# Performance work log

Measured on AMD Instinct MI355X. Metric: run time of the kernel, lower is better.

## Reference

```python
import jax, jax.numpy as jnp
import numpy as np

N_NODES = 50000
N_EDGES = 800000
D_IN = 128
D_HID = 128   # initlial_net_sizes[-1]
D_GC = 128    # gc_out
D_OUT = 256   # feats_out


def setup_inputs() -> dict:
    key = jax.random.key(0)
    ks = jax.random.split(key, 8)
    feats = jax.random.normal(ks[0], (N_NODES, D_IN), dtype=jnp.float32)
    edges = jax.random.randint(ks[1], (2, N_EDGES), 0, N_NODES, dtype=jnp.int64)
    batch = jnp.sort(jax.random.randint(ks[2], (N_NODES,), 0, 64, dtype=jnp.int64))
    s = 0.05
    W1 = jax.random.normal(ks[3], (D_IN, D_HID), dtype=jnp.float32) * s
    b1 = jnp.zeros((D_HID,), dtype=jnp.float32)
    Wg = jax.random.normal(ks[4], (D_HID, D_GC), dtype=jnp.float32) * s
    bg = jnp.zeros((D_GC,), dtype=jnp.float32)
    W2 = jax.random.normal(ks[5], (D_HID + D_GC, D_OUT), dtype=jnp.float32) * s
    b2 = jnp.zeros((D_OUT,), dtype=jnp.float32)
    return {"feats": feats, "edges": edges, "batch": batch,
            "W1": W1, "b1": b1, "Wg": Wg, "bg": bg, "W2": W2, "b2": b2}


def _gcn_conv(x, edges, Wg, bg):
    # PyG GCNConv: linear -> add self-loops -> sym degree norm -> scatter-add -> bias
    n = x.shape[0]
    x = x @ Wg                                   # [N, D_GC]
    loop = jnp.arange(n, dtype=edges.dtype)
    src = jnp.concatenate([edges[0], loop])      # message source (x_j)
    dst = jnp.concatenate([edges[1], loop])      # aggregation target
    deg = jax.ops.segment_sum(jnp.ones_like(dst, dtype=x.dtype), dst, num_segments=n)
    dinv = jnp.where(deg > 0, jax.lax.rsqrt(deg), 0.0)
    norm = dinv[src] * dinv[dst]                 # [E+N]
    msg = x[src] * norm[:, None]                 # [E+N, D_GC]
    out = jax.ops.segment_sum(msg, dst, num_segments=n)
    return out + bg


def reference(feats, edges, batch, W1, b1, Wg, bg, W2, b2):
    nfeats = feats @ W1 + b1                     # fcnn (single Linear, no activation)
    gc_feats = _gcn_conv(nfeats, edges, Wg, bg)  # GCNConv
    combined = jnp.concatenate([nfeats, gc_feats], axis=1) @ W2 + b2
    return (combined, edges, batch)
```

## Files before the change

### kernel.cpp

```cpp
#include <hip/hip_runtime.h>
#include <hip/hip_bf16.h>
#include <stdint.h>


#define NND 50000
#define NE  800000

typedef unsigned int u32;
typedef unsigned short u16;
typedef unsigned long long u64;
typedef short bf16x8 __attribute__((ext_vector_type(8)));
typedef float f32x4  __attribute__((ext_vector_type(4)));

#define OFF_CSR  12800000
#define OFF_RNK  13200000
#define OFF_ROW  13600000
#define OFF_DEG  13700004
#define OFF_DINV 13750004
#define OFF_WPK2 13800004
#define OFF_WPK1 13832772
#define OFF_WPKG 13840964

__device__ __forceinline__ float bf_lo(u32 u) { return __uint_as_float(u << 16); }
__device__ __forceinline__ float bf_hi(u32 u) { return __uint_as_float(u & 0xFFFF0000u); }
__device__ __forceinline__ unsigned short f2b(float f) {
    __hip_bfloat16 h = __float2bfloat16(f);
    return *(unsigned short*)&h;
}
__device__ __forceinline__ u32 pk2(float lo, float hi) {
    return ((u32)f2b(hi) << 16) | (u32)f2b(lo);
}

__device__ __forceinline__ int probe_isbf_par(const u32* p, int stride, int lane) {
    u32 v = p[lane * stride];
    u32 e = (v >> 7) & 0xFFu;
    u64 m = __ballot(e >= 90u && e <= 150u);
    return (__popcll(m) >= 40) ? 1 : 0;
}
__device__ __forceinline__ int probe_intfmt_par(const u32* p, int base, int stride, int lane) {
    int i = lane & 31;
    bool lo = lane < 32;
    u32 a = p[base + i * stride];
    u32 b = p[base + i * stride + 1];
    u32 e1 = (a >> 7) & 0xFFu;
    int small = __popcll(__ballot(lo && a < 50000u))
              + __popcll(__ballot(lo && b < 50000u));
    int oddz  = __popcll(__ballot(lo && b == 0u));
    int bfe   = __popcll(__ballot(lo && e1 >= 110u && e1 <= 145u));
    return (small >= 56) ? ((oddz >= 31) ? 1 : 0) : ((bfe >= 20) ? 3 : 2);
}

__device__ __forceinline__ int iread(const void* p, int fmt, int idx) {
    switch (fmt) {
        case 0:  return ((const int*)p)[idx];
        case 1:  return ((const int*)p)[2 * idx];
        case 2:  return (int)(((const float*)p)[idx] + 0.5f);
        default: return (int)(__bfloat162float(((const __hip_bfloat16*)p)[idx]) + 0.5f);
    }
}
__device__ __forceinline__ float fread_pass(const void* p, int fmt, int idx) {
    switch (fmt) {
        case 0:  return (float)((const int*)p)[idx];
        case 1:  return (float)((const int*)p)[2 * idx];
        case 2:  return ((const float*)p)[idx];
        default: return __bfloat162float(((const __hip_bfloat16*)p)[idx]);
    }
}
__device__ __forceinline__ float rdf(const void* p, int idx, int isbf) {
    return isbf ? __bfloat162float(((const __hip_bfloat16*)p)[idx])
                : ((const float*)p)[idx];
}
__device__ __forceinline__ float rdbias(const void* p, int idx) {
    return __bfloat162float(((const __hip_bfloat16*)p)[idx]);
}

__global__ __launch_bounds__(256) void k_pack(
    const void* W1, const void* Wg, const void* W2,
    u16* __restrict__ Wpk1, u16* __restrict__ Wpkg, u16* __restrict__ Wpk2,
    int* __restrict__ deg)
{
    int b = blockIdx.x, tid = threadIdx.x, lane = tid & 63;
    if (b < 64) {
        int wbf = probe_isbf_par((const u32*)W1, 127, lane);
        int idx = b * 256 + tid;
        int j = idx & 7, l = (idx >> 3) & 63, nt = (idx >> 9) & 7, kk = (idx >> 12) & 3;
        int k = kk * 32 + ((l >> 4) & 3) * 8 + j;
        int n = nt * 16 + (l & 15);
        Wpk1[idx] = f2b(rdf(W1, k * 128 + n, wbf));
    } else if (b < 128) {
        int wbf = probe_isbf_par((const u32*)Wg, 127, lane);
        int idx = (b - 64) * 256 + tid;
        int j = idx & 7, l = (idx >> 3) & 63, nt = (idx >> 9) & 7, kk = (idx >> 12) & 3;
        int k = kk * 32 + ((l >> 4) & 3) * 8 + j;
        int n = nt * 16 + (l & 15);
        Wpkg[idx] = f2b(rdf(Wg, k * 128 + n, wbf));
    } else if (b < 384) {
        int wbf = probe_isbf_par((const u32*)W2, 509, lane);
        int idx = (b - 128) * 256 + tid;
        int j = idx & 7, l = (idx >> 3) & 63, nt = (idx >> 9) & 15, kk = idx >> 13;
        int k = kk * 32 + ((l >> 4) & 3) * 8 + j;
        int n = nt * 16 + (l & 15);
        Wpk2[idx] = f2b(rdf(W2, k * 256 + n, wbf));
    } else {
        int idx = (b - 384) * 256 + tid;
        if (idx < 12500) ((int4*)deg)[idx] = make_int4(0, 0, 0, 0);
    }
}

__global__ __launch_bounds__(256) void k_degnfxp(
    const void* edges, const void* feats,
    const u32* __restrict__ Wpk1, const u32* __restrict__ Wpkg, const void* b1,
    int* __restrict__ deg, u16* __restrict__ rank16,
    float* __restrict__ out, int M)
{
    __shared__ alignas(16) u32 smem[2048 + 2176];
    int b = blockIdx.x, tid = threadIdx.x, lane = tid & 63;

    if (b < 3125) {
        int fmt = probe_intfmt_par((const u32*)edges, 0, 24992, lane);
        int e = b * 256 + tid;
        if (e < NE) {
            int s = iread(edges, fmt, e);
            int d = iread(edges, fmt, NE + e);
            if ((u32)s < (u32)NND && (u32)d < (u32)NND) {
                int r = atomicAdd(&deg[d], 1);
                rank16[e] = (u16)r;
            }
        }
        return;
    }

    int nb = b - 3125;
    int row0 = nb * 32;
    int w = tid >> 6;
    u32* sApk = smem;
    uint4* sApk4 = (uint4*)smem;
    u16* nfl  = (u16*)(smem + 2048);

    int fbf = probe_isbf_par((const u32*)feats, 997, lane);

    if (fbf) {
        const u32* fw = (const u32*)feats;
        for (int i4 = tid; i4 < 512; i4 += 256) {
            int l = i4 & 63, kk = (i4 >> 6) & 3, mt = (i4 >> 8) & 1;
            int m = mt * 16 + (l & 15);
            int k0b = kk * 32 + ((l >> 4) & 3) * 8;
            int row = row0 + m;
            uint4 v = make_uint4(0u, 0u, 0u, 0u);
            if (row < M) v = *(const uint4*)&fw[(size_t)row * 64 + (k0b >> 1)];
            sApk4[i4] = v;
        }
    } else {
        const float* ff = (const float*)feats;
        for (int i4 = tid; i4 < 512; i4 += 256) {
            int l = i4 & 63, kk = (i4 >> 6) & 3, mt = (i4 >> 8) & 1;
            int m = mt * 16 + (l & 15);
            int k0b = kk * 32 + ((l >> 4) & 3) * 8;
            int row = row0 + m;
            uint4 v = make_uint4(0u, 0u, 0u, 0u);
            if (row < M) {
                float4 fa = *(const float4*)&ff[(size_t)row * 128 + k0b];
                float4 fb = *(const float4*)&ff[(size_t)row * 128 + k0b + 4];
                v = make_uint4(pk2(fa.x, fa.y), pk2(fa.z, fa.w),
                               pk2(fb.x, fb.y), pk2(fb.z, fb.w));
            }
            sApk4[i4] = v;
        }
    }
    __syncthreads();

    f32x4 acc[2][2];
#pragma unroll
    for (int mt = 0; mt < 2; ++mt)
#pragma unroll
        for (int t = 0; t < 2; ++t) acc[mt][t] = (f32x4){0.f, 0.f, 0.f, 0.f};

    for (int kk = 0; kk < 4; ++kk) {
        union { uint4 u; bf16x8 h; } ca0, ca1;
        ca0.u = *(const uint4*)&sApk[(kk * 64 + lane) * 4];
        ca1.u = *(const uint4*)&sApk[((4 + kk) * 64 + lane) * 4];
#pragma unroll
        for (int t = 0; t < 2; ++t) {
            int nt = w * 2 + t;
            union { uint4 u; bf16x8 h; } cb;
            cb.u = *(const uint4*)&Wpk1[((kk * 8 + nt) * 64 + lane) * 4];
            acc[0][t] = __builtin_amdgcn_mfma_f32_16x16x32_bf16(ca0.h, cb.h, acc[0][t], 0, 0, 0);
            acc[1][t] = __builtin_amdgcn_mfma_f32_16x16x32_bf16(ca1.h, cb.h, acc[1][t], 0, 0, 0);
        }
    }

    unsigned short* o16 = (unsigned short*)out;
    int q = lane >> 4, cn = lane & 15;
#pragma unroll
    for (int mt = 0; mt < 2; ++mt)
#pragma unroll
        for (int t = 0; t < 2; ++t) {
            int col = (w * 2 + t) * 16 + cn;
            float bb = rdbias(b1, col);
#pragma unroll
            for (int r = 0; r < 4; ++r) {
                int rowl = mt * 16 + q * 4 + r;
                int row = row0 + rowl;
                unsigned short v = f2b(acc[mt][t][r] + bb);
                nfl[rowl * 136 + col] = v;
                if (row < M) o16[(size_t)row * 512 + col] = v;
            }
        }
    __syncthreads();

    f32x4 acc2[2][2];
#pragma unroll
    for (int mt = 0; mt < 2; ++mt)
#pragma unroll
        for (int t = 0; t < 2; ++t) acc2[mt][t] = (f32x4){0.f, 0.f, 0.f, 0.f};

    for (int kk = 0; kk < 4; ++kk) {
        int kcol = kk * 32 + ((lane >> 4) & 3) * 8;
        union { uint4 u; bf16x8 h; } ca0, ca1;
        ca0.u = *(const uint4*)&nfl[(lane & 15) * 136 + kcol];
        ca1.u = *(const uint4*)&nfl[(16 + (lane & 15)) * 136 + kcol];
#pragma unroll
        for (int t = 0; t < 2; ++t) {
            int nt = w * 2 + t;
            union { uint4 u; bf16x8 h; } cb;
            cb.u = *(const uint4*)&Wpkg[((kk * 8 + nt) * 64 + lane) * 4];
            acc2[0][t] = __builtin_amdgcn_mfma_f32_16x16x32_bf16(ca0.h, cb.h, acc2[0][t], 0, 0, 0);
            acc2[1][t] = __builtin_amdgcn_mfma_f32_16x16x32_bf16(ca1.h, cb.h, acc2[1][t], 0, 0, 0);
        }
    }

#pragma unroll
    for (int mt = 0; mt < 2; ++mt)
#pragma unroll
        for (int t = 0; t < 2; ++t) {
            int col = (w * 2 + t) * 16 + cn;
#pragma unroll
            for (int r = 0; r < 4; ++r) {
                int row = row0 + mt * 16 + q * 4 + r;
                if (row < M)
                    o16[(size_t)row * 512 + 256 + col] = f2b(acc2[mt][t][r]);
            }
        }
}

__global__ __launch_bounds__(256) void k_scan(
    const int* __restrict__ deg,
    int* __restrict__ row_start, float* __restrict__ dinv)
{
    __shared__ int part[256];
    __shared__ int stot;
    int t = threadIdx.x, b = blockIdx.x;

    int acc = 0;
    for (int c = 0; c < b; ++c) acc += deg[c * 256 + t];
    part[t] = acc;
    __syncthreads();
    for (int off = 128; off >= 1; off >>= 1) {
        if (t < off) part[t] += part[t + off];
        __syncthreads();
    }
    if (t == 0) stot = part[0];
    __syncthreads();
    int S_b = stot;
    __syncthreads();

    int idx = b * 256 + t;
    int dv = (idx < NND) ? deg[idx] : 0;
    part[t] = dv;
    __syncthreads();
    for (int off = 1; off < 256; off <<= 1) {
        int x = (t >= off) ? part[t - off] : 0;
        __syncthreads();
        part[t] += x;
        __syncthreads();
    }
    if (idx < NND) {
        int rs = S_b + part[t] - dv;
        row_start[idx] = rs;
        dinv[idx] = rsqrtf((float)(dv + 1));
    }
    if (b == 195 && t == 255) row_start[NND] = S_b + part[255];
}

__global__ __launch_bounds__(256) void k_place(const void* edges,
                                               const int* __restrict__ row_start,
                                               const u16* __restrict__ rank16,
                                               u16* __restrict__ csr16)
{
    int fmt = probe_intfmt_par((const u32*)edges, 0, 24992, threadIdx.x & 63);
    int e = blockIdx.x * 256 + threadIdx.x;
    if (e < NE) {
        int s = iread(edges, fmt, e);
        int d = iread(edges, fmt, NE + e);
        if ((u32)s < (u32)NND && (u32)d < (u32)NND) {
            int pos = row_start[d] + (int)rank16[e];
            csr16[pos] = (u16)s;
        }
    }
}

__global__ __launch_bounds__(256) void k_gather(
    const u16* __restrict__ csr16, const int* __restrict__ row_start,
    const float* __restrict__ dinv, const void* bg, u32* __restrict__ uw)
{
    int gt = blockIdx.x * 256 + threadIdx.x;
    int node = gt >> 6, l = gt & 63;
    if (node >= NND) return;
    int beg = row_start[node], end = row_start[node + 1];

    u32 us = uw[(size_t)node * 256 + 128 + l];
    float di = dinv[node];
    float bg0 = rdbias(bg, 2 * l);
    float bg1 = rdbias(bg, 2 * l + 1);

    float a0 = 0.f, a1 = 0.f;
    float c0 = 0.f, c1 = 0.f;
    int e0 = end - 1;
    for (int i = beg; i < end; i += 8) {
        int j1 = i + 1, j2 = i + 2, j3 = i + 3;
        int j4 = i + 4, j5 = i + 5, j6 = i + 6, j7 = i + 7;
        int s0 = csr16[i];
        int s1 = csr16[j1 < e0 ? j1 : e0];
        int s2 = csr16[j2 < e0 ? j2 : e0];
        int s3 = csr16[j3 < e0 ? j3 : e0];
        int s4 = csr16[j4 < e0 ? j4 : e0];
        int s5 = csr16[j5 < e0 ? j5 : e0];
        int s6 = csr16[j6 < e0 ? j6 : e0];
        int s7 = csr16[j7 < e0 ? j7 : e0];
        u32 u0 = uw[(size_t)s0 * 256 + 128 + l];
        u32 u1 = uw[(size_t)s1 * 256 + 128 + l];
        u32 u2 = uw[(size_t)s2 * 256 + 128 + l];
        u32 u3 = uw[(size_t)s3 * 256 + 128 + l];
        u32 u4 = uw[(size_t)s4 * 256 + 128 + l];
        u32 u5 = uw[(size_t)s5 * 256 + 128 + l];
        u32 u6 = uw[(size_t)s6 * 256 + 128 + l];
        u32 u7 = uw[(size_t)s7 * 256 + 128 + l];
        float w0 = dinv[s0];
        float w1 = (j1 <= e0) ? dinv[s1] : 0.f;
        float w2 = (j2 <= e0) ? dinv[s2] : 0.f;
        float w3 = (j3 <= e0) ? dinv[s3] : 0.f;
        float w4 = (j4 <= e0) ? dinv[s4] : 0.f;
        float w5 = (j5 <= e0) ? dinv[s5] : 0.f;
        float w6 = (j6 <= e0) ? dinv[s6] : 0.f;
        float w7 = (j7 <= e0) ? dinv[s7] : 0.f;
        a0 = fmaf(w0, bf_lo(u0), a0); a1 = fmaf(w0, bf_hi(u0), a1);
        c0 = fmaf(w1, bf_lo(u1), c0); c1 = fmaf(w1, bf_hi(u1), c1);
        a0 = fmaf(w2, bf_lo(u2), a0); a1 = fmaf(w2, bf_hi(u2), a1);
        c0 = fmaf(w3, bf_lo(u3), c0); c1 = fmaf(w3, bf_hi(u3), c1);
        a0 = fmaf(w4, bf_lo(u4), a0); a1 = fmaf(w4, bf_hi(u4), a1);
        c0 = fmaf(w5, bf_lo(u5), c0); c1 = fmaf(w5, bf_hi(u5), c1);
        a0 = fmaf(w6, bf_lo(u6), a0); a1 = fmaf(w6, bf_hi(u6), a1);
        c0 = fmaf(w7, bf_lo(u7), c0); c1 = fmaf(w7, bf_hi(u7), c1);
    }
    a0 += c0; a1 += c1;
    float g0 = di * (a0 + di * bf_lo(us)) + bg0;
    float g1 = di * (a1 + di * bf_hi(us)) + bg1;
    uw[(size_t)node * 256 + 192 + l] = ((u32)f2b(g1) << 16) | (u32)f2b(g0);
}

__global__ __launch_bounds__(256) void k_final(
    const u32* __restrict__ Wpk, const void* b2, float* __restrict__ out, int M)
{
    __shared__ alignas(16) u32 sApk[4096];
    uint4* sApk4 = (uint4*)sApk;
    int tid = threadIdx.x;
    int row0 = blockIdx.x * 32;
    const u32* uw = (const u32*)out;

    for (int i4 = tid; i4 < 1024; i4 += 256) {
        int l = i4 & 63, kk = (i4 >> 6) & 7, mt = (i4 >> 9) & 1;
        int m = mt * 16 + (l & 15);
        int k0b = kk * 32 + ((l >> 4) & 3) * 8;
        int row = row0 + m;
        uint4 v = make_uint4(0u, 0u, 0u, 0u);
        if (row < M) {
            size_t base = (kk < 4)
                ? (size_t)row * 256 + (k0b >> 1)
                : (size_t)row * 256 + 192 + ((k0b - 128) >> 1);
            v = *(const uint4*)&uw[base];
        }
        sApk4[i4] = v;
    }
    __syncthreads();

    int w = tid >> 6, lane = tid & 63;
    f32x4 acc[2][4];
#pragma unroll
    for (int mt = 0; mt < 2; ++mt)
#pragma unroll
        for (int t = 0; t < 4; ++t) acc[mt][t] = (f32x4){0.f, 0.f, 0.f, 0.f};

    for (int kk = 0; kk < 8; ++kk) {
        union { uint4 u; bf16x8 h; } ca0, ca1;
        ca0.u = *(const uint4*)&sApk[(kk * 64 + lane) * 4];
        ca1.u = *(const uint4*)&sApk[((8 + kk) * 64 + lane) * 4];
#pragma unroll
        for (int t = 0; t < 4; ++t) {
            int nt = w * 4 + t;
            union { uint4 u; bf16x8 h; } cb;
            cb.u = *(const uint4*)&Wpk[((size_t)(kk * 16 + nt) * 64 + lane) * 4];
            acc[0][t] = __builtin_amdgcn_mfma_f32_16x16x32_bf16(ca0.h, cb.h, acc[0][t], 0, 0, 0);
            acc[1][t] = __builtin_amdgcn_mfma_f32_16x16x32_bf16(ca1.h, cb.h, acc[1][t], 0, 0, 0);
        }
    }

    int q = lane >> 4, cn = lane & 15;
#pragma unroll
    for (int mt = 0; mt < 2; ++mt)
#pragma unroll
        for (int t = 0; t < 4; ++t) {
            int col = w * 64 + t * 16 + cn;
            float bb = rdbias(b2, col);
#pragma unroll
            for (int r = 0; r < 4; ++r) {
                int row = row0 + mt * 16 + q * 4 + r;
                if (row < M) {
                    float v = acc[mt][t][r] + bb;
                    if (!(fabsf(v) < 900.f)) v = (v == v) ? copysignf(900.f, v) : 0.f;
                    out[(size_t)row * 256 + col] = v;
                }
            }
        }
}

__global__ __launch_bounds__(256) void k_tail(
    const void* edges, const void* batch, float* __restrict__ out)
{
    int lane = threadIdx.x & 63;
    int f0 = probe_intfmt_par((const u32*)edges, 0, 24992, lane);
    int f1 = probe_intfmt_par((const u32*)batch, 20000, 156, lane);
    int T = blockIdx.x * 256 + threadIdx.x;
    if (T < NE) {
        size_t o = (size_t)NND * 256 + 2 * (size_t)T;
        if (f0 == 1) {
            int4 v = ((const int4*)edges)[T];
            *(float2*)&out[o] = make_float2((float)v.x, (float)v.z);
        } else {
            out[o]     = fread_pass(edges, f0, 2 * T);
            out[o + 1] = fread_pass(edges, f0, 2 * T + 1);
        }
    } else if (T < NE + NND / 2) {
        int U = T - NE;
        size_t o = (size_t)NND * 256 + 2 * (size_t)NE + 2 * (size_t)U;
        if (f1 == 1) {
            int4 v = ((const int4*)batch)[U];
            *(float2*)&out[o] = make_float2((float)v.x, (float)v.z);
        } else {
            out[o]     = fread_pass(batch, f1, 2 * U);
            out[o + 1] = fread_pass(batch, f1, 2 * U + 1);
        }
    }
}

extern "C" void kernel_launch(void* const* d_in, const int* in_sizes, int n_in,
                              void* d_out, int out_size, void* d_ws, size_t ws_size,
                              hipStream_t stream)
{
    int i_feats = -1, i_edges = -1, i_batch = -1, i_W1 = -1, i_Wg = -1,
        i_W2 = -1, i_b1 = -1, i_bg = -1, i_b2 = -1;
    for (int i = 0; i < n_in; ++i) {
        int s = in_sizes[i];
        if      (s == 6400000) i_feats = i;
        else if (s == 1600000) i_edges = i;
        else if (s == 50000)   i_batch = i;
        else if (s == 65536)   i_W2 = i;
        else if (s == 256)     i_b2 = i;
        else if (s == 16384)   { if (i_W1 < 0) i_W1 = i; else i_Wg = i; }
        else if (s == 128)     { if (i_b1 < 0) i_b1 = i; else i_bg = i; }
    }
    if (i_feats < 0 || i_edges < 0 || i_batch < 0 || i_W1 < 0 || i_Wg < 0 ||
        i_W2 < 0 || i_b1 < 0 || i_bg < 0 || i_b2 < 0) {
        i_feats = 0; i_edges = 1; i_batch = 2; i_W1 = 3; i_b1 = 4;
        i_Wg = 5; i_bg = 6; i_W2 = 7; i_b2 = 8;
    }
    const void* feats = d_in[i_feats];
    const void* edges = d_in[i_edges];
    const void* batch = d_in[i_batch];
    const void* W1 = d_in[i_W1];
    const void* b1 = d_in[i_b1];
    const void* Wg = d_in[i_Wg];
    const void* bg = d_in[i_bg];
    const void* W2 = d_in[i_W2];
    const void* b2 = d_in[i_b2];

    float* out = (float*)d_out;
    u16*   csr16     = (u16*)  (out + OFF_CSR);
    u16*   rank16    = (u16*)  (out + OFF_RNK);
    int*   row_start = (int*)  (out + OFF_ROW);
    int*   deg       = (int*)  (out + OFF_DEG);
    float* dinv      = (float*)(out + OFF_DINV);
    u16*   Wpk2 = (u16*)(out + OFF_WPK2);
    u16*   Wpk1 = (u16*)(out + OFF_WPK1);
    u16*   Wpkg = (u16*)(out + OFF_WPKG);

    k_pack    <<<433,   256, 0, stream>>>(W1, Wg, W2, Wpk1, Wpkg, Wpk2, deg);
    k_degnfxp <<<4688,  256, 0, stream>>>(edges, feats, (const u32*)Wpk1,
                                          (const u32*)Wpkg, b1, deg, rank16,
                                          out, NND);
    k_scan    <<<196,   256, 0, stream>>>(deg, row_start, dinv);
    k_place   <<<3125,  256, 0, stream>>>(edges, row_start, rank16, csr16);
    k_gather  <<<12500, 256, 0, stream>>>(csr16, row_start, dinv, bg, (u32*)out);
    k_final   <<<1563,  256, 0, stream>>>((const u32*)Wpk2, b2, out, NND);
    k_tail    <<<3224,  256, 0, stream>>>(edges, batch, out);
}
```

Before: 248.7 us.

## Interleave degree and GEMM blocks, vectorize placement, fuse final GEMM with tail copy

```diff
diff --git a/kernel.cpp b/kernel.cpp
--- a/kernel.cpp
+++ b/kernel.cpp
@@ -20,6 +20,9 @@
 #define OFF_WPK2 13800004
 #define OFF_WPK1 13832772
 #define OFF_WPKG 13840964
+
+#define GUARD_LO 500002
+#define GUARD_HI 516386
 
 __device__ __forceinline__ float bf_lo(u32 u) { return __uint_as_float(u << 16); }
 __device__ __forceinline__ float bf_hi(u32 u) { return __uint_as_float(u & 0xFFFF0000u); }
@@ -115,23 +118,25 @@
 {
     __shared__ alignas(16) u32 smem[2048 + 2176];
     int b = blockIdx.x, tid = threadIdx.x, lane = tid & 63;
-
-    if (b < 3125) {
+    int q = b / 3, r = b - 3 * q;
+
+    if (r != 2) {
+        int db = 2 * q + r;
+        if (db >= 3125) return;
         int fmt = probe_intfmt_par((const u32*)edges, 0, 24992, lane);
-        int e = b * 256 + tid;
+        int e = db * 256 + tid;
         if (e < NE) {
             int s = iread(edges, fmt, e);
             int d = iread(edges, fmt, NE + e);
             if ((u32)s < (u32)NND && (u32)d < (u32)NND) {
-                int r = atomicAdd(&deg[d], 1);
-                rank16[e] = (u16)r;
+                int rk = atomicAdd(&deg[d], 1);
+                rank16[e] = (u16)rk;
             }
         }
         return;
     }
 
-    int nb = b - 3125;
-    int row0 = nb * 32;
+    int row0 = q * 32;
     int w = tid >> 6;
     u32* sApk = smem;
     uint4* sApk4 = (uint4*)smem;
@@ -190,7 +195,7 @@
     }
 
     unsigned short* o16 = (unsigned short*)out;
-    int q = lane >> 4, cn = lane & 15;
+    int qq = lane >> 4, cn = lane & 15;
 #pragma unroll
     for (int mt = 0; mt < 2; ++mt)
 #pragma unroll
@@ -198,10 +203,10 @@
             int col = (w * 2 + t) * 16 + cn;
             float bb = rdbias(b1, col);
 #pragma unroll
-            for (int r = 0; r < 4; ++r) {
-                int rowl = mt * 16 + q * 4 + r;
+            for (int rr = 0; rr < 4; ++rr) {
+                int rowl = mt * 16 + qq * 4 + rr;
                 int row = row0 + rowl;
-                unsigned short v = f2b(acc[mt][t][r] + bb);
+                unsigned short v = f2b(acc[mt][t][rr] + bb);
                 nfl[rowl * 136 + col] = v;
                 if (row < M) o16[(size_t)row * 512 + col] = v;
             }
@@ -235,10 +240,10 @@
         for (int t = 0; t < 2; ++t) {
             int col = (w * 2 + t) * 16 + cn;
 #pragma unroll
-            for (int r = 0; r < 4; ++r) {
-                int row = row0 + mt * 16 + q * 4 + r;
+            for (int rr = 0; rr < 4; ++rr) {
+                int row = row0 + mt * 16 + qq * 4 + rr;
                 if (row < M)
-                    o16[(size_t)row * 512 + 256 + col] = f2b(acc2[mt][t][r]);
+                    o16[(size_t)row * 512 + 256 + col] = f2b(acc2[mt][t][rr]);
             }
         }
 }
@@ -287,16 +292,25 @@
                                                const u16* __restrict__ rank16,
                                                u16* __restrict__ csr16)
 {
-    int fmt = probe_intfmt_par((const u32*)edges, 0, 24992, threadIdx.x & 63);
-    int e = blockIdx.x * 256 + threadIdx.x;
-    if (e < NE) {
-        int s = iread(edges, fmt, e);
-        int d = iread(edges, fmt, NE + e);
-        if ((u32)s < (u32)NND && (u32)d < (u32)NND) {
-            int pos = row_start[d] + (int)rank16[e];
-            csr16[pos] = (u16)s;
-        }
-    }
+    int lane = threadIdx.x & 63;
+    int fmt = probe_intfmt_par((const u32*)edges, 0, 24992, lane);
+    int T = blockIdx.x * 256 + threadIdx.x;
+    if (T >= NE / 2) return;
+    int e0 = 2 * T, e1 = 2 * T + 1;
+    int s0, d0, s1, d1;
+    if (fmt == 1) {
+        int4 sv = ((const int4*)edges)[T];
+        int4 dv = ((const int4*)edges)[NE / 2 + T];
+        s0 = sv.x; s1 = sv.z; d0 = dv.x; d1 = dv.z;
+    } else {
+        s0 = iread(edges, fmt, e0); d0 = iread(edges, fmt, NE + e0);
+        s1 = iread(edges, fmt, e1); d1 = iread(edges, fmt, NE + e1);
+    }
+    u32 rr = *(const u32*)&rank16[e0];
+    if ((u32)s0 < (u32)NND && (u32)d0 < (u32)NND)
+        csr16[row_start[d0] + (int)(rr & 0xFFFFu)] = (u16)s0;
+    if ((u32)s1 < (u32)NND && (u32)d1 < (u32)NND)
+        csr16[row_start[d1] + (int)(rr >> 16)] = (u16)s1;
 }
 
 __global__ __launch_bounds__(256) void k_gather(
@@ -358,13 +372,44 @@
     uw[(size_t)node * 256 + 192 + l] = ((u32)f2b(g1) << 16) | (u32)f2b(g0);
 }
 
-__global__ __launch_bounds__(256) void k_final(
-    const u32* __restrict__ Wpk, const void* b2, float* __restrict__ out, int M)
+__global__ __launch_bounds__(256) void k_finaltail(
+    const u32* __restrict__ Wpk, const void* b2,
+    const void* edges, const void* batch, float* __restrict__ out, int M)
 {
     __shared__ alignas(16) u32 sApk[4096];
+    int bb = blockIdx.x, tid = threadIdx.x;
+
+    if (bb >= 1563) {
+        int lane = tid & 63;
+        int f0 = probe_intfmt_par((const u32*)edges, 0, 24992, lane);
+        int f1 = probe_intfmt_par((const u32*)batch, 20000, 156, lane);
+        int T = (bb - 1563) * 256 + tid;
+        if (T < NE) {
+            if (T >= GUARD_LO && T < GUARD_HI) return;
+            size_t o = (size_t)NND * 256 + 2 * (size_t)T;
+            if (f0 == 1) {
+                int4 v = ((const int4*)edges)[T];
+                *(float2*)&out[o] = make_float2((float)v.x, (float)v.z);
+            } else {
+                out[o]     = fread_pass(edges, f0, 2 * T);
+                out[o + 1] = fread_pass(edges, f0, 2 * T + 1);
+            }
+        } else if (T < NE + NND / 2) {
+            int U = T - NE;
+            size_t o = (size_t)NND * 256 + 2 * (size_t)NE + 2 * (size_t)U;
+            if (f1 == 1) {
+                int4 v = ((const int4*)batch)[U];
+                *(float2*)&out[o] = make_float2((float)v.x, (float)v.z);
+            } else {
+                out[o]     = fread_pass(batch, f1, 2 * U);
+                out[o + 1] = fread_pass(batch, f1, 2 * U + 1);
+            }
+        }
+        return;
+    }
+
     uint4* sApk4 = (uint4*)sApk;
-    int tid = threadIdx.x;
-    int row0 = blockIdx.x * 32;
+    int row0 = bb * 32;
     const u32* uw = (const u32*)out;
 
     for (int i4 = tid; i4 < 1024; i4 += 256) {
@@ -410,12 +455,12 @@
 #pragma unroll
         for (int t = 0; t < 4; ++t) {
             int col = w * 64 + t * 16 + cn;
-            float bb = rdbias(b2, col);
+            float bb2 = rdbias(b2, col);
 #pragma unroll
             for (int r = 0; r < 4; ++r) {
                 int row = row0 + mt * 16 + q * 4 + r;
                 if (row < M) {
-                    float v = acc[mt][t][r] + bb;
+                    float v = acc[mt][t][r] + bb2;
                     if (!(fabsf(v) < 900.f)) v = (v == v) ? copysignf(900.f, v) : 0.f;
                     out[(size_t)row * 256 + col] = v;
                 }
@@ -423,32 +468,19 @@
         }
 }
 
-__global__ __launch_bounds__(256) void k_tail(
-    const void* edges, const void* batch, float* __restrict__ out)
+__global__ __launch_bounds__(256) void k_patch(
+    const void* edges, float* __restrict__ out)
 {
     int lane = threadIdx.x & 63;
     int f0 = probe_intfmt_par((const u32*)edges, 0, 24992, lane);
-    int f1 = probe_intfmt_par((const u32*)batch, 20000, 156, lane);
-    int T = blockIdx.x * 256 + threadIdx.x;
-    if (T < NE) {
-        size_t o = (size_t)NND * 256 + 2 * (size_t)T;
-        if (f0 == 1) {
-            int4 v = ((const int4*)edges)[T];
-            *(float2*)&out[o] = make_float2((float)v.x, (float)v.z);
-        } else {
-            out[o]     = fread_pass(edges, f0, 2 * T);
-            out[o + 1] = fread_pass(edges, f0, 2 * T + 1);
-        }
-    } else if (T < NE + NND / 2) {
-        int U = T - NE;
-        size_t o = (size_t)NND * 256 + 2 * (size_t)NE + 2 * (size_t)U;
-        if (f1 == 1) {
-            int4 v = ((const int4*)batch)[U];
-            *(float2*)&out[o] = make_float2((float)v.x, (float)v.z);
-        } else {
-            out[o]     = fread_pass(batch, f1, 2 * U);
-            out[o + 1] = fread_pass(batch, f1, 2 * U + 1);
-        }
+    int T = GUARD_LO + blockIdx.x * 256 + threadIdx.x;
+    size_t o = (size_t)NND * 256 + 2 * (size_t)T;
+    if (f0 == 1) {
+        int4 v = ((const int4*)edges)[T];
+        *(float2*)&out[o] = make_float2((float)v.x, (float)v.z);
+    } else {
+        out[o]     = fread_pass(edges, f0, 2 * T);
+        out[o + 1] = fread_pass(edges, f0, 2 * T + 1);
     }
 }
 
@@ -493,13 +525,14 @@
     u16*   Wpk1 = (u16*)(out + OFF_WPK1);
     u16*   Wpkg = (u16*)(out + OFF_WPKG);
 
-    k_pack    <<<433,   256, 0, stream>>>(W1, Wg, W2, Wpk1, Wpkg, Wpk2, deg);
-    k_degnfxp <<<4688,  256, 0, stream>>>(edges, feats, (const u32*)Wpk1,
-                                          (const u32*)Wpkg, b1, deg, rank16,
-                                          out, NND);
-    k_scan    <<<196,   256, 0, stream>>>(deg, row_start, dinv);
-    k_place   <<<3125,  256, 0, stream>>>(edges, row_start, rank16, csr16);
-    k_gather  <<<12500, 256, 0, stream>>>(csr16, row_start, dinv, bg, (u32*)out);
-    k_final   <<<1563,  256, 0, stream>>>((const u32*)Wpk2, b2, out, NND);
-    k_tail    <<<3224,  256, 0, stream>>>(edges, batch, out);
-}
+    k_pack     <<<433,   256, 0, stream>>>(W1, Wg, W2, Wpk1, Wpkg, Wpk2, deg);
+    k_degnfxp  <<<4689,  256, 0, stream>>>(edges, feats, (const u32*)Wpk1,
+                                           (const u32*)Wpkg, b1, deg, rank16,
+                                           out, NND);
+    k_scan     <<<196,   256, 0, stream>>>(deg, row_start, dinv);
+    k_place    <<<1563,  256, 0, stream>>>(edges, row_start, rank16, csr16);
+    k_gather   <<<12500, 256, 0, stream>>>(csr16, row_start, dinv, bg, (u32*)out);
+    k_finaltail<<<4787,  256, 0, stream>>>((const u32*)Wpk2, b2, edges, batch,
+                                           out, NND);
+    k_patch    <<<64,    256, 0, stream>>>(edges, out);
+}
```

Result: faster. 235.3 us (-5.4%).
